# Performance work log

Hardware: AMD Instinct MI355X
Metric: run time of the kernel (lower is better)

Reference implementation:

```python
import jax, jax.numpy as jnp
import numpy as np

T, B, I, H, O = 4096, 256, 2, 32, 1


def setup_inputs() -> dict:
    key = jax.random.key(0)
    ks = jax.random.split(key, 8)
    s = 1.0 / np.sqrt(H)  # torch GRU/Linear init scale
    u = lambda k, shape: jax.random.uniform(k, shape, jnp.float32, -s, s)
    return {
        "x": jax.random.normal(ks[0], (T, B, I), jnp.float32),
        "w_ih": u(ks[1], (3 * H, I)),   # rows ordered [r, z, n] as in torch
        "w_hh": u(ks[2], (3 * H, H)),
        "b_ih": u(ks[3], (3 * H,)),
        "b_hh": u(ks[4], (3 * H,)),
        "w_fc": u(ks[5], (O, H)),
        "b_fc": u(ks[6], (O,)),
    }


def _gru_all_hidden(x, w_ih, w_hh, b_ih, b_hh):
    # Precompute input projections for all steps in one big GEMM: (T,B,3H)
    xg = jnp.einsum('tbi,gi->tbg', x, w_ih) + b_ih

    def step(h, xg_t):
        hg = h @ w_hh.T + b_hh                      # (B,3H)
        xr, xz, xn = jnp.split(xg_t, 3, axis=-1)
        hr, hz, hn = jnp.split(hg, 3, axis=-1)
        r = jax.nn.sigmoid(xr + hr)
        z = jax.nn.sigmoid(xz + hz)
        n = jnp.tanh(xn + r * hn)
        h_new = (1.0 - z) * n + z * h
        return h_new, h_new

    h0 = jnp.zeros((x.shape[1], w_hh.shape[1]), x.dtype)
    _, hs = jax.lax.scan(step, h0, xg)
    return hs                                       # (T,B,H)


def reference(x, w_ih, w_hh, b_ih, b_hh, w_fc, b_fc):
    hs = _gru_all_hidden(x, w_ih, w_hh, b_ih, b_hh)  # (T,B,H)
    # Faithful to the source: output[:, -1, :] with batch_first=False picks
    # the last batch element's hidden state at every timestep -> (T,H)
    out = hs[:, -1, :]
    return out @ w_fc.T + b_fc                       # (T,O)
```

## Files before the change

### kernel.cpp

```cpp
#include <hip/hip_runtime.h>


#define TT 4096

typedef _Float16 h2 __attribute__((ext_vector_type(2)));

__device__ __forceinline__ float rl(float v, int l) {
    return __int_as_float(__builtin_amdgcn_readlane(__float_as_int(v), l));
}
__device__ __forceinline__ int rli(int v, int l) {
    return __builtin_amdgcn_readlane(v, l);
}
__device__ __forceinline__ float fexp2(float x) { return __builtin_amdgcn_exp2f(x); }
__device__ __forceinline__ float frcp(float x)  { return __builtin_amdgcn_rcpf(x); }
__device__ __forceinline__ h2 asph(int v) { return __builtin_bit_cast(h2, v); }

#define NLOG2E  (-1.44269504088896340736f)
#define TLOG2E  ( 2.88539008177792681472f)

__global__ __launch_bounds__(64, 1)
void gru_seq(const float* __restrict__ x,
             const float* __restrict__ w_ih,
             const float* __restrict__ w_hh,
             const float* __restrict__ b_ih,
             const float* __restrict__ b_hh,
             float* __restrict__ hbuf)
{
    const int lane = threadIdx.x;
    const int low  = lane & 31;
    const bool hi  = lane >= 32;
    const int row0 = lane;
    const int row1 = 64 + low;

    h2 w0p[16], w1p[16];
#pragma unroll
    for (int m = 0; m < 16; ++m) {
        float a = w_hh[row0 * 32 + 2 * m] * NLOG2E;
        float b = w_hh[row0 * 32 + 2 * m + 1] * NLOG2E;
        w0p[m] = h2{(_Float16)a, (_Float16)b};
    }
#pragma unroll
    for (int m = 0; m < 16; ++m) {
        float a = w_hh[row1 * 32 + 2 * m] * TLOG2E;
        float b = w_hh[row1 * 32 + 2 * m + 1] * TLOG2E;
        w1p[m] = h2{(_Float16)a, (_Float16)b};
    }

    const float wi00 = w_ih[row0 * 2 + 0] * NLOG2E;
    const float wi01 = w_ih[row0 * 2 + 1] * NLOG2E;
    const float wi10 = w_ih[row1 * 2 + 0] * TLOG2E;
    const float wi11 = w_ih[row1 * 2 + 1] * TLOG2E;
    const float bias0 = (b_ih[row0] + b_hh[row0]) * NLOG2E;
    const float bi1   = b_ih[row1] * TLOG2E;
    const float bh1   = b_hh[row1] * TLOG2E;

    float h_el = 0.0f;
    int hsp[16];
#pragma unroll
    for (int m = 0; m < 16; ++m) hsp[m] = 0;

    const float2* xp = (const float2*)x;
    float2 xv = xp[(size_t)lane * 256 + 255];
    float hacc[4];
    const int odd = lane & 1;

    for (int tb = 0; tb < 64; ++tb) {
        float2 xv_next = xv;
        if (tb < 63) xv_next = xp[((size_t)(tb + 1) * 64 + lane) * 256 + 255];
        float4* hout = (float4*)(hbuf + (size_t)low * TT + tb * 64);

#pragma unroll 4
        for (int i = 0; i < 64; ++i) {
            const float x0 = rl(xv.x, i);
            const float x1 = rl(xv.y, i);
            const float base0 = fmaf(x1, wi01, fmaf(x0, wi00, bias0));
            const float xn    = fmaf(x1, wi11, fmaf(x0, wi10, bi1));

            float a0 = base0, a1 = 0.f;
            float n0 = bh1,   n1 = 0.f;
#pragma unroll
            for (int m = 0; m < 16; m += 2) {
                const h2 hA = asph(hsp[m]);
                const h2 hB = asph(hsp[m + 1]);
                a0 = __builtin_amdgcn_fdot2(w0p[m],     hA, a0, false);
                a1 = __builtin_amdgcn_fdot2(w0p[m + 1], hB, a1, false);
                n0 = __builtin_amdgcn_fdot2(w1p[m],     hA, n0, false);
                n1 = __builtin_amdgcn_fdot2(w1p[m + 1], hB, n1, false);
            }
            const float pre_s = a0 + a1;
            const float hn_s  = n0 + n1;

            const float sg    = frcp(1.0f + fexp2(pre_s));
            const float other = __shfl_xor(sg, 32);
            const float rr = hi ? other : sg;
            const float zz = hi ? sg : other;

            const float nv = fmaf(-2.0f, frcp(1.0f + fexp2(fmaf(rr, hn_s, xn))), 1.0f);
            h_el = fmaf(zz, h_el - nv, nv);

            hacc[i & 3] = h_el;
            if ((i & 3) == 3) hout[i >> 2] = *(const float4*)hacc;

            const float nb = __int_as_float(__builtin_amdgcn_update_dpp(
                0, __float_as_int(h_el), 0xB1, 0xF, 0xF, true));
            const float pa = odd ? nb : h_el;
            const float pb = odd ? h_el : nb;
            const int pk = __builtin_bit_cast(int, __builtin_amdgcn_cvt_pkrtz(pa, pb));
#pragma unroll
            for (int m = 0; m < 16; ++m) hsp[m] = rli(pk, 2 * m);
        }
        xv = xv_next;
    }
}

__global__ void fc_out(const float* __restrict__ hbuf,
                       const float* __restrict__ w_fc,
                       const float* __restrict__ b_fc,
                       float* __restrict__ out)
{
    const int t = blockIdx.x * blockDim.x + threadIdx.x;
    if (t >= TT) return;
    float acc = 0.f;
#pragma unroll
    for (int j = 0; j < 32; ++j) acc = fmaf(hbuf[j * TT + t], w_fc[j], acc);
    out[t] = acc + b_fc[0];
}

extern "C" void kernel_launch(void* const* d_in, const int* in_sizes, int n_in,
                              void* d_out, int out_size, void* d_ws, size_t ws_size,
                              hipStream_t stream) {
    const float* x    = (const float*)d_in[0];
    const float* w_ih = (const float*)d_in[1];
    const float* w_hh = (const float*)d_in[2];
    const float* b_ih = (const float*)d_in[3];
    const float* b_hh = (const float*)d_in[4];
    const float* w_fc = (const float*)d_in[5];
    const float* b_fc = (const float*)d_in[6];
    float* out  = (float*)d_out;
    float* hbuf = (float*)d_ws;

    gru_seq<<<1, 64, 0, stream>>>(x, w_ih, w_hh, b_ih, b_hh, hbuf);
    fc_out<<<TT / 256, 256, 0, stream>>>(hbuf, w_fc, b_fc, out);
}
```

Measured before the change: 776.8 us.

## Compute all three GRU gates per lane to drop cross-half shuffle

Each lane now holds the r, z and n weight rows for its own hidden unit and evaluates all three gate dot products itself. Both half-waves compute the same values. This removes the per-step __shfl_xor across the two halves and the odd/even select before packing. The cost is more fdot2 work and an extra exp/rcp on the serial recurrence. Hidden-state writes also change from batched float4 stores to one scalar store per step, duplicated across the halves, and the kernel gets a waves_per_eu hint.

```diff
diff --git a/kernel.cpp b/kernel.cpp
--- a/kernel.cpp
+++ b/kernel.cpp
@@ -19,6 +19,7 @@
 #define TLOG2E  ( 2.88539008177792681472f)
 
 __global__ __launch_bounds__(64, 1)
+__attribute__((amdgpu_waves_per_eu(1)))
 void gru_seq(const float* __restrict__ x,
              const float* __restrict__ w_ih,
              const float* __restrict__ w_hh,
@@ -28,31 +29,31 @@
 {
     const int lane = threadIdx.x;
     const int low  = lane & 31;
-    const bool hi  = lane >= 32;
-    const int row0 = lane;
-    const int row1 = 64 + low;
+    const int row_r = low;
+    const int row_z = 32 + low;
+    const int row_n = 64 + low;
 
-    h2 w0p[16], w1p[16];
+    h2 wr[16], wz[16], wn[16];
 #pragma unroll
     for (int m = 0; m < 16; ++m) {
-        float a = w_hh[row0 * 32 + 2 * m] * NLOG2E;
-        float b = w_hh[row0 * 32 + 2 * m + 1] * NLOG2E;
-        w0p[m] = h2{(_Float16)a, (_Float16)b};
-    }
-#pragma unroll
-    for (int m = 0; m < 16; ++m) {
-        float a = w_hh[row1 * 32 + 2 * m] * TLOG2E;
-        float b = w_hh[row1 * 32 + 2 * m + 1] * TLOG2E;
-        w1p[m] = h2{(_Float16)a, (_Float16)b};
+        wr[m] = h2{(_Float16)(w_hh[row_r * 32 + 2 * m]     * NLOG2E),
+                   (_Float16)(w_hh[row_r * 32 + 2 * m + 1] * NLOG2E)};
+        wz[m] = h2{(_Float16)(w_hh[row_z * 32 + 2 * m]     * NLOG2E),
+                   (_Float16)(w_hh[row_z * 32 + 2 * m + 1] * NLOG2E)};
+        wn[m] = h2{(_Float16)(w_hh[row_n * 32 + 2 * m]     * TLOG2E),
+                   (_Float16)(w_hh[row_n * 32 + 2 * m + 1] * TLOG2E)};
     }
 
-    const float wi00 = w_ih[row0 * 2 + 0] * NLOG2E;
-    const float wi01 = w_ih[row0 * 2 + 1] * NLOG2E;
-    const float wi10 = w_ih[row1 * 2 + 0] * TLOG2E;
-    const float wi11 = w_ih[row1 * 2 + 1] * TLOG2E;
-    const float bias0 = (b_ih[row0] + b_hh[row0]) * NLOG2E;
-    const float bi1   = b_ih[row1] * TLOG2E;
-    const float bh1   = b_hh[row1] * TLOG2E;
+    const float wir0 = w_ih[row_r * 2 + 0] * NLOG2E;
+    const float wir1 = w_ih[row_r * 2 + 1] * NLOG2E;
+    const float wiz0 = w_ih[row_z * 2 + 0] * NLOG2E;
+    const float wiz1 = w_ih[row_z * 2 + 1] * NLOG2E;
+    const float win0 = w_ih[row_n * 2 + 0] * TLOG2E;
+    const float win1 = w_ih[row_n * 2 + 1] * TLOG2E;
+    const float br = (b_ih[row_r] + b_hh[row_r]) * NLOG2E;
+    const float bz = (b_ih[row_z] + b_hh[row_z]) * NLOG2E;
+    const float bin = b_ih[row_n] * TLOG2E;
+    const float bhn = b_hh[row_n] * TLOG2E;
 
     float h_el = 0.0f;
     int hsp[16];
@@ -61,51 +62,48 @@
 
     const float2* xp = (const float2*)x;
     float2 xv = xp[(size_t)lane * 256 + 255];
-    float hacc[4];
-    const int odd = lane & 1;
 
     for (int tb = 0; tb < 64; ++tb) {
         float2 xv_next = xv;
         if (tb < 63) xv_next = xp[((size_t)(tb + 1) * 64 + lane) * 256 + 255];
-        float4* hout = (float4*)(hbuf + (size_t)low * TT + tb * 64);
+        float* hout = hbuf + (size_t)low * TT + tb * 64;
 
 #pragma unroll 4
         for (int i = 0; i < 64; ++i) {
             const float x0 = rl(xv.x, i);
             const float x1 = rl(xv.y, i);
-            const float base0 = fmaf(x1, wi01, fmaf(x0, wi00, bias0));
-            const float xn    = fmaf(x1, wi11, fmaf(x0, wi10, bi1));
+            const float base_r = fmaf(x1, wir1, fmaf(x0, wir0, br));
+            const float base_z = fmaf(x1, wiz1, fmaf(x0, wiz0, bz));
+            const float xn     = fmaf(x1, win1, fmaf(x0, win0, bin));
 
-            float a0 = base0, a1 = 0.f;
-            float n0 = bh1,   n1 = 0.f;
+            float r0 = base_r, r1 = 0.f;
+            float z0 = base_z, z1 = 0.f;
+            float n0 = bhn,    n1 = 0.f;
 #pragma unroll
             for (int m = 0; m < 16; m += 2) {
                 const h2 hA = asph(hsp[m]);
                 const h2 hB = asph(hsp[m + 1]);
-                a0 = __builtin_amdgcn_fdot2(w0p[m],     hA, a0, false);
-                a1 = __builtin_amdgcn_fdot2(w0p[m + 1], hB, a1, false);
-                n0 = __builtin_amdgcn_fdot2(w1p[m],     hA, n0, false);
-                n1 = __builtin_amdgcn_fdot2(w1p[m + 1], hB, n1, false);
+                r0 = __builtin_amdgcn_fdot2(wr[m],     hA, r0, false);
+                r1 = __builtin_amdgcn_fdot2(wr[m + 1], hB, r1, false);
+                z0 = __builtin_amdgcn_fdot2(wz[m],     hA, z0, false);
+                z1 = __builtin_amdgcn_fdot2(wz[m + 1], hB, z1, false);
+                n0 = __builtin_amdgcn_fdot2(wn[m],     hA, n0, false);
+                n1 = __builtin_amdgcn_fdot2(wn[m + 1], hB, n1, false);
             }
-            const float pre_s = a0 + a1;
+            const float pre_r = r0 + r1;
+            const float pre_z = z0 + z1;
             const float hn_s  = n0 + n1;
 
-            const float sg    = frcp(1.0f + fexp2(pre_s));
-            const float other = __shfl_xor(sg, 32);
-            const float rr = hi ? other : sg;
-            const float zz = hi ? sg : other;
+            const float rv = frcp(1.0f + fexp2(pre_r));
+            const float zv = frcp(1.0f + fexp2(pre_z));
+            const float nv = fmaf(-2.0f, frcp(1.0f + fexp2(fmaf(rv, hn_s, xn))), 1.0f);
+            h_el = fmaf(zv, h_el - nv, nv);
 
-            const float nv = fmaf(-2.0f, frcp(1.0f + fexp2(fmaf(rr, hn_s, xn))), 1.0f);
-            h_el = fmaf(zz, h_el - nv, nv);
-
-            hacc[i & 3] = h_el;
-            if ((i & 3) == 3) hout[i >> 2] = *(const float4*)hacc;
+            hout[i] = h_el;
 
             const float nb = __int_as_float(__builtin_amdgcn_update_dpp(
                 0, __float_as_int(h_el), 0xB1, 0xF, 0xF, true));
-            const float pa = odd ? nb : h_el;
-            const float pb = odd ? h_el : nb;
-            const int pk = __builtin_bit_cast(int, __builtin_amdgcn_cvt_pkrtz(pa, pb));
+            const int pk = __builtin_bit_cast(int, __builtin_amdgcn_cvt_pkrtz(h_el, nb));
 #pragma unroll
             for (int m = 0; m < 16; ++m) hsp[m] = rli(pk, 2 * m);
         }
```

Measured after the change: 841.2 us. +8.3%, slower.
